# Optimization experiments

Measured on AMD Instinct MI355X. Metric: run time of the kernel, lower is better.

## Reference

```python
import jax, jax.numpy as jnp
import numpy as np

NUM_HEADS = 16

def setup_inputs() -> dict:
    key = jax.random.key(0)
    ks = jax.random.split(key, 10)
    B, S, D = 2, 2048, 1024
    q = jax.random.normal(ks[0], (B, S, D), dtype=jnp.float32)
    k = jax.random.normal(ks[1], (B, S, D), dtype=jnp.float32)
    v = jax.random.normal(ks[2], (B, S, D), dtype=jnp.float32)
    mask = jax.random.randint(ks[3], (B, S), 0, 2, dtype=jnp.int32)
    scale = 0.02
    Wq = jax.random.normal(ks[4], (D, D), dtype=jnp.float32) * scale
    bq = jax.random.normal(ks[5], (D,), dtype=jnp.float32) * scale
    Wk = jax.random.normal(ks[6], (D, D), dtype=jnp.float32) * scale
    bk = jax.random.normal(ks[7], (D,), dtype=jnp.float32) * scale
    Wv = jax.random.normal(ks[8], (D, D), dtype=jnp.float32) * scale
    bv = jax.random.normal(ks[9], (D,), dtype=jnp.float32) * scale
    return {"q": q, "k": k, "v": v, "mask": mask,
            "Wq": Wq, "bq": bq, "Wk": Wk, "bk": bk, "Wv": Wv, "bv": bv}


def reference(q, k, v, mask, Wq, bq, Wk, bk, Wv, bv):
    B, S, D = q.shape
    H = NUM_HEADS
    dh = D // H
    # per-head split along last dim == reshape to (B, S, H, dh)
    Qh = (q @ Wq + bq).reshape(B, S, H, dh)
    Kh = (k @ Wk + bk).reshape(B, S, H, dh)
    Vh = (v @ Wv + bv).reshape(B, S, H, dh)
    # NOTE: original scales by sqrt(10), not sqrt(dim_per_head)
    scores = jnp.einsum('bqhd,bkhd->bhqk', Qh, Kh) / jnp.sqrt(jnp.float32(10.0))
    # mask [B,S] masks key positions; masked_fill replaces with -1e9
    scores = jnp.where(mask[:, None, None, :] == 0, jnp.float32(-1e9), scores)
    probs = jax.nn.softmax(scores, axis=-1)
    out = jnp.einsum('bhqk,bkhd->bqhd', probs, Vh).reshape(B, S, D)
    return out
```

## Files before the change

kernel.cpp:

```cpp
#include <hip/hip_runtime.h>
#include <hip/hip_bf16.h>

typedef __attribute__((ext_vector_type(8))) short short8;
typedef __attribute__((ext_vector_type(4))) float f32x4;

#define SC_L2E 0.4561727848849353f

#if __has_builtin(__builtin_amdgcn_exp2f)
#define EXP2F __builtin_amdgcn_exp2f
#else
#define EXP2F exp2f
#endif

static __device__ __forceinline__ void gload16(const void* g, void* l) {
  __builtin_amdgcn_global_load_lds((const __attribute__((address_space(1))) void*)g,
                                   (__attribute__((address_space(3))) void*)l, 16, 0, 0);
}

__global__ void k_cvt(const float* __restrict__ q, const float* __restrict__ kk,
                      const float* __restrict__ v, __hip_bfloat16* __restrict__ xb,
                      const float* __restrict__ Wq, const float* __restrict__ Wk,
                      const float* __restrict__ Wv, __hip_bfloat16* __restrict__ wt,
                      const int* __restrict__ mask, float* __restrict__ bias2) {
  __shared__ float T[64][65];
  if (blockIdx.x < 6144) {
    const size_t i = ((size_t)blockIdx.x * 256 + threadIdx.x) * 8;
    const int t = (int)(i >> 22);
    const float* src = (t == 0) ? q : (t == 1) ? kk : v;
    const size_t off = i & 4194303u;
    float4 f0 = *(const float4*)(src + off);
    float4 f1 = *(const float4*)(src + off + 4);
    union { short8 s; __hip_bfloat16 h[8]; } u;
    u.h[0] = __float2bfloat16(f0.x); u.h[1] = __float2bfloat16(f0.y);
    u.h[2] = __float2bfloat16(f0.z); u.h[3] = __float2bfloat16(f0.w);
    u.h[4] = __float2bfloat16(f1.x); u.h[5] = __float2bfloat16(f1.y);
    u.h[6] = __float2bfloat16(f1.z); u.h[7] = __float2bfloat16(f1.w);
    *(short8*)((char*)xb + i * 2) = u.s;
    return;
  }
  const int idx2 = blockIdx.x - 6144;
  const int z = idx2 >> 8;
  const int r2 = idx2 & 255;
  const int bxi = r2 & 15, byi = r2 >> 4;
  if (z == 0 && byi == 0) {
    const int idx = bxi * 256 + threadIdx.x;
    bias2[idx] = mask[idx] ? -12.0f : -1e30f;
  }
  const float* W = (z == 0) ? Wq : (z == 1) ? Wk : Wv;
  __hip_bfloat16* Wd = wt + (size_t)z * 1048576;
  const int n0 = bxi * 64, k0 = byi * 64;
  const int tx = threadIdx.x & 63, ty = threadIdx.x >> 6;
#pragma unroll
  for (int r = 0; r < 16; ++r)
    T[ty + r * 4][tx] = W[(size_t)(k0 + ty + r * 4) * 1024 + n0 + tx];
  __syncthreads();
#pragma unroll
  for (int r = 0; r < 16; ++r)
    Wd[(size_t)(n0 + ty + r * 4) * 1024 + k0 + tx] = __float2bfloat16(T[tx][ty + r * 4]);
}

__global__ __launch_bounds__(256) void k_proj(
    const __hip_bfloat16* __restrict__ xb, const __hip_bfloat16* __restrict__ wt,
    const float* __restrict__ bq, const float* __restrict__ bk, const float* __restrict__ bv,
    __hip_bfloat16* __restrict__ Qb, __hip_bfloat16* __restrict__ Kb,
    __hip_bfloat16* __restrict__ Vt) {
  __shared__ char smem[32768];
  char* As = smem;
  char* Bs = smem + 16384;
  const int orig = blockIdx.x;
  const int xcd = orig & 7, idx = orig >> 3;
  const int by = xcd * 4 + (idx & 3);
  const int bx = (idx >> 2) & 7;
  const int t = idx >> 5;
  const char* X = (const char*)(xb + (size_t)t * 4194304);
  const char* W = (const char*)(wt + (size_t)t * 1048576);
  const float* bias = (t == 0) ? bq : (t == 1) ? bk : bv;
  const int m0 = by * 128, n0 = bx * 128;
  const int tid = threadIdx.x, w = tid >> 6, lane = tid & 63;
  const int l15 = lane & 15, g = lane >> 4;
  const int l8 = lane >> 3, l7 = lane & 7;
  const int vswz = ((l7 ^ l8) << 4);
  const int wm = (w >> 1) * 64, wn = (w & 1) * 64;
  f32x4 acc[4][4];
#pragma unroll
  for (int i = 0; i < 4; ++i)
#pragma unroll
    for (int j = 0; j < 4; ++j) acc[i][j] = (f32x4){0.f, 0.f, 0.f, 0.f};

  for (int k0 = 0; k0 < 2048; k0 += 128) {
    __syncthreads();
#pragma unroll
    for (int j = 0; j < 4; ++j) {
      const int ch = w * 4 + j;
      gload16(X + (size_t)(m0 + ch * 8 + l8) * 2048 + k0 + vswz, As + ch * 1024);
      gload16(W + (size_t)(n0 + ch * 8 + l8) * 2048 + k0 + vswz, Bs + ch * 1024);
    }
    __syncthreads();
#pragma unroll
    for (int kk = 0; kk < 2; ++kk) {
      short8 af[4], bf_[4];
#pragma unroll
      for (int mt = 0; mt < 4; ++mt) {
        const int row = wm + mt * 16 + l15;
        af[mt] = *(const short8*)(As + row * 128 + ((kk * 64 + g * 16) ^ ((row & 7) << 4)));
      }
#pragma unroll
      for (int nt = 0; nt < 4; ++nt) {
        const int row = wn + nt * 16 + l15;
        bf_[nt] = *(const short8*)(Bs + row * 128 + ((kk * 64 + g * 16) ^ ((row & 7) << 4)));
      }
#pragma unroll
      for (int mt = 0; mt < 4; ++mt)
#pragma unroll
        for (int nt = 0; nt < 4; ++nt)
          acc[mt][nt] = __builtin_amdgcn_mfma_f32_16x16x32_bf16(af[mt], bf_[nt], acc[mt][nt], 0, 0, 0);
    }
  }

  float bv4[4];
#pragma unroll
  for (int nt = 0; nt < 4; ++nt) bv4[nt] = bias[n0 + wn + nt * 16 + l15];

  if (t < 2) {
#pragma unroll
    for (int mt = 0; mt < 4; ++mt) {
#pragma unroll
      for (int nt = 0; nt < 4; ++nt) {
        const int feat = n0 + wn + nt * 16 + l15;
        const int h = feat >> 6, d = feat & 63;
#pragma unroll
        for (int r = 0; r < 4; ++r) {
          const int token = m0 + wm + mt * 16 + g * 4 + r;
          const int b = token >> 11, s = token & 2047;
          const float val = acc[mt][nt][r] + bv4[nt];
          const __hip_bfloat16 hb = __float2bfloat16(val);
          if (t == 0) Qb[((size_t)(b * 16 + h) * 2048 + s) * 64 + d] = hb;
          else        Kb[((size_t)(b * 16 + h) * 2048 + s) * 64 + d] = hb;
        }
      }
    }
  } else {
    __hip_bfloat16* T2 = (__hip_bfloat16*)smem;
    const int bb = m0 >> 11;
    const int s0 = m0 & 2047;
#pragma unroll
    for (int p = 0; p < 2; ++p) {
      __syncthreads();
      if ((w >> 1) == p) {
#pragma unroll
        for (int mt = 0; mt < 4; ++mt)
#pragma unroll
          for (int nt = 0; nt < 4; ++nt) {
            const int feat = wn + nt * 16 + l15;
#pragma unroll
            for (int r = 0; r < 4; ++r) {
              const int tok = mt * 16 + g * 4 + r;
              T2[feat * 64 + (tok ^ ((feat & 7) << 3))] =
                  __float2bfloat16(acc[mt][nt][r] + bv4[nt]);
            }
          }
      }
      __syncthreads();
#pragma unroll
      for (int sw = 0; sw < 4; ++sw) {
        const int row = sw * 32 + (tid >> 3);
        const int c = tid & 7;
        const short8 vchunk = *(const short8*)(smem + row * 128 + 16 * (c ^ (row & 7)));
        const int gfeat = n0 + row;
        const int hh = gfeat >> 6, dd = gfeat & 63;
        *(short8*)(Vt + ((size_t)((bb * 16 + hh) * 64 + dd)) * 2048 + s0 + p * 64 + c * 8) = vchunk;
      }
    }
  }
}

#define ATTN_BODY(CUR, NXT, PREF)                                              \
  {                                                                            \
    float4 mb[4];                                                              \
    _Pragma("unroll") for (int nt = 0; nt < 4; ++nt)                           \
        mb[nt] = *(const float4*)(mbp + (nt >> 1) * 32 + ((nt & 1) << 2) + g * 8); \
    mbp += 64;                                                                 \
    if (PREF) {                                                                \
      _Pragma("unroll") for (int j = 0; j < 2; ++j) {                          \
        gload16(kst[j], Ks[NXT] + (w * 2 + j) * 1024);                         \
        gload16(vst[j], Vs[NXT] + (w * 2 + j) * 1024);                         \
      }                                                                        \
    }                                                                          \
    kst[0] += 8192; kst[1] += 8192; vst[0] += 128; vst[1] += 128;              \
    f32x4 s_[4];                                                               \
    __builtin_amdgcn_s_setprio(1);                                             \
    _Pragma("unroll") for (int nt = 0; nt < 4; ++nt) {                         \
      s_[nt] = (f32x4){0.f, 0.f, 0.f, 0.f};                                    \
      const int key = nt * 16 + l15;                                           \
      _Pragma("unroll") for (int kc = 0; kc < 2; ++kc) {                       \
        const short8 kf = *(const short8*)(Ks[CUR] + key * 128 +               \
                           ((kc * 64 + g * 16) ^ ((key & 7) << 4)));           \
        s_[nt] = __builtin_amdgcn_mfma_f32_16x16x32_bf16(kf, aq[kc], s_[nt], 0, 0, 0); \
      }                                                                        \
    }                                                                          \
    __builtin_amdgcn_s_setprio(0);                                             \
    short8 pb8[2];                                                             \
    _Pragma("unroll") for (int c = 0; c < 2; ++c) {                            \
      union { short8 s8; __hip_bfloat16 hh[8]; } pu;                           \
      pu.hh[0] = __float2bfloat16(EXP2F(fmaf(s_[2*c][0], SC_L2E, mb[2*c].x))); \
      pu.hh[1] = __float2bfloat16(EXP2F(fmaf(s_[2*c][1], SC_L2E, mb[2*c].y))); \
      pu.hh[2] = __float2bfloat16(EXP2F(fmaf(s_[2*c][2], SC_L2E, mb[2*c].z))); \
      pu.hh[3] = __float2bfloat16(EXP2F(fmaf(s_[2*c][3], SC_L2E, mb[2*c].w))); \
      pu.hh[4] = __float2bfloat16(EXP2F(fmaf(s_[2*c+1][0], SC_L2E, mb[2*c+1].x))); \
      pu.hh[5] = __float2bfloat16(EXP2F(fmaf(s_[2*c+1][1], SC_L2E, mb[2*c+1].y))); \
      pu.hh[6] = __float2bfloat16(EXP2F(fmaf(s_[2*c+1][2], SC_L2E, mb[2*c+1].z))); \
      pu.hh[7] = __float2bfloat16(EXP2F(fmaf(s_[2*c+1][3], SC_L2E, mb[2*c+1].w))); \
      pb8[c] = pu.s8;                                                          \
    }                                                                          \
    __builtin_amdgcn_s_setprio(1);                                             \
    lacc = __builtin_amdgcn_mfma_f32_16x16x32_bf16(ones8, pb8[0], lacc, 0, 0, 0); \
    lacc = __builtin_amdgcn_mfma_f32_16x16x32_bf16(ones8, pb8[1], lacc, 0, 0, 0); \
    _Pragma("unroll") for (int dt = 0; dt < 4; ++dt) {                         \
      const int d = dt * 16 + l15;                                             \
      const int sw2 = (d & 7) << 4;                                            \
      f32x4 o = oaccT[dt];                                                     \
      const short8 v0 = *(const short8*)(Vs[CUR] + d * 128 + ((g * 16) ^ sw2)); \
      const short8 v1 = *(const short8*)(Vs[CUR] + d * 128 + ((64 + g * 16) ^ sw2)); \
      o = __builtin_amdgcn_mfma_f32_16x16x32_bf16(v0, pb8[0], o, 0, 0, 0);     \
      o = __builtin_amdgcn_mfma_f32_16x16x32_bf16(v1, pb8[1], o, 0, 0, 0);     \
      oaccT[dt] = o;                                                           \
    }                                                                          \
    __builtin_amdgcn_s_setprio(0);                                             \
    __syncthreads();                                                           \
  }

__global__ __launch_bounds__(256, 4) void k_attn(
    const __hip_bfloat16* __restrict__ Qb, const __hip_bfloat16* __restrict__ Kb,
    const __hip_bfloat16* __restrict__ Vt, const float* __restrict__ bias2,
    float* __restrict__ out) {
  __shared__ char Ks[2][8192];
  __shared__ char Vs[2][8192];
  const int orig = blockIdx.x;
  const int swz = (orig & 7) * 128 + (orig >> 3);
  const int bh = swz >> 5, qb = swz & 31;
  const int b = bh >> 4, h = bh & 15;
  const int tid = threadIdx.x, w = tid >> 6, lane = tid & 63;
  const int g = lane >> 4, l15 = lane & 15;
  const char* Qc = (const char*)(Qb + (size_t)bh * 131072);
  const char* Kc = (const char*)(Kb + (size_t)bh * 131072);
  const char* Vc = (const char*)(Vt + (size_t)bh * 131072);

  const int l8 = lane >> 3, l7 = lane & 7;
  const int vswz = ((l7 ^ l8) << 4);

  short8 aq[2];
  const int arow = qb * 64 + w * 16 + l15;
#pragma unroll
  for (int kc = 0; kc < 2; ++kc)
    aq[kc] = *(const short8*)(Qc + (size_t)arow * 128 + kc * 64 + g * 16);

  f32x4 oaccT[4];
#pragma unroll
  for (int i = 0; i < 4; ++i) oaccT[i] = (f32x4){0.f, 0.f, 0.f, 0.f};
  f32x4 lacc = (f32x4){0.f, 0.f, 0.f, 0.f};
  const short8 ones8 = {(short)0x3F80, (short)0x3F80, (short)0x3F80, (short)0x3F80,
                        (short)0x3F80, (short)0x3F80, (short)0x3F80, (short)0x3F80};

  const char* kst[2];
  const char* vst[2];
#pragma unroll
  for (int j = 0; j < 2; ++j) {
    const int ch = w * 2 + j;
    const int s = ch * 8 + l8;
    const int nt = s >> 4, gg = (s >> 2) & 3, rr = s & 3;
    const int kap = (nt >> 1) * 32 + gg * 8 + ((nt & 1) << 2) + rr;
    kst[j] = Kc + (size_t)kap * 128 + vswz;
    vst[j] = Vc + (size_t)s * 4096 + vswz;
    gload16(kst[j], Ks[0] + ch * 1024);
    gload16(vst[j], Vs[0] + ch * 1024);
    kst[j] += 8192;
    vst[j] += 128;
  }
  __syncthreads();

  const float* mbp = bias2 + b * 2048;
  for (int kt = 0; kt < 32; kt += 2) {
    ATTN_BODY(0, 1, true)
    ATTN_BODY(1, 0, (kt + 1 < 31))
  }

  const float rl = 1.0f / lacc[0];
  float* orow = out + ((size_t)(b * 2048 + arow)) * 1024 + h * 64;
#pragma unroll
  for (int dt = 0; dt < 4; ++dt) {
    float4 st;
    st.x = oaccT[dt][0] * rl; st.y = oaccT[dt][1] * rl;
    st.z = oaccT[dt][2] * rl; st.w = oaccT[dt][3] * rl;
    *(float4*)(orow + dt * 16 + g * 4) = st;
  }
}

extern "C" void kernel_launch(void* const* d_in, const int* in_sizes, int n_in,
                              void* d_out, int out_size, void* d_ws, size_t ws_size,
                              hipStream_t stream) {
  const float* q   = (const float*)d_in[0];
  const float* k   = (const float*)d_in[1];
  const float* v   = (const float*)d_in[2];
  const int* mask  = (const int*)d_in[3];
  const float* Wq  = (const float*)d_in[4];
  const float* bq  = (const float*)d_in[5];
  const float* Wk  = (const float*)d_in[6];
  const float* bk  = (const float*)d_in[7];
  const float* Wv  = (const float*)d_in[8];
  const float* bv  = (const float*)d_in[9];
  float* out = (float*)d_out;
  char* ws = (char*)d_ws;
  __hip_bfloat16* Xb = (__hip_bfloat16*)(ws);
  __hip_bfloat16* Wt = (__hip_bfloat16*)(ws + 25165824);
  __hip_bfloat16* Qb = (__hip_bfloat16*)(ws + 31457280);
  __hip_bfloat16* Kb = (__hip_bfloat16*)(ws + 39845888);
  __hip_bfloat16* Vt = (__hip_bfloat16*)(ws + 48234496);
  float* bias2      = (float*)(ws + 56623104);

  k_cvt<<<dim3(6912), dim3(256), 0, stream>>>(q, k, v, Xb, Wq, Wk, Wv, Wt, mask, bias2);
  k_proj<<<dim3(768), dim3(256), 0, stream>>>(Xb, Wt, bq, bk, bv, Qb, Kb, Vt);
  k_attn<<<dim3(1024), dim3(256), 0, stream>>>(Qb, Kb, Vt, bias2, out);
}
```

Measured before the change: 109.8 us.

## Double attention query tile to 128 rows with 8 waves per block

The attention kernel now launches 512 blocks of 512 threads. Each block covers 128 query rows instead of 64, and the K/V tile loads are spread over 8 waves, one 16-byte chunk per wave instead of two. This halves the total K/V global-to-LDS traffic and the number of blocks streaming the same head's keys and values. In exchange, more waves share each barrier per tile, and there are fewer blocks to spread across the CUs.

```diff
diff --git a/kernel.cpp b/kernel.cpp
--- a/kernel.cpp
+++ b/kernel.cpp
@@ -181,12 +181,10 @@
         mb[nt] = *(const float4*)(mbp + (nt >> 1) * 32 + ((nt & 1) << 2) + g * 8); \
     mbp += 64;                                                                 \
     if (PREF) {                                                                \
-      _Pragma("unroll") for (int j = 0; j < 2; ++j) {                          \
-        gload16(kst[j], Ks[NXT] + (w * 2 + j) * 1024);                         \
-        gload16(vst[j], Vs[NXT] + (w * 2 + j) * 1024);                         \
-      }                                                                        \
+      gload16(kst, Ks[NXT] + w * 1024);                                        \
+      gload16(vst, Vs[NXT] + w * 1024);                                        \
     }                                                                          \
-    kst[0] += 8192; kst[1] += 8192; vst[0] += 128; vst[1] += 128;              \
+    kst += 8192; vst += 128;                                                   \
     f32x4 s_[4];                                                               \
     __builtin_amdgcn_s_setprio(1);                                             \
     _Pragma("unroll") for (int nt = 0; nt < 4; ++nt) {                         \
@@ -229,15 +227,15 @@
     __syncthreads();                                                           \
   }
 
-__global__ __launch_bounds__(256, 4) void k_attn(
+__global__ __launch_bounds__(512, 2) void k_attn(
     const __hip_bfloat16* __restrict__ Qb, const __hip_bfloat16* __restrict__ Kb,
     const __hip_bfloat16* __restrict__ Vt, const float* __restrict__ bias2,
     float* __restrict__ out) {
   __shared__ char Ks[2][8192];
   __shared__ char Vs[2][8192];
   const int orig = blockIdx.x;
-  const int swz = (orig & 7) * 128 + (orig >> 3);
-  const int bh = swz >> 5, qb = swz & 31;
+  const int swz = (orig & 7) * 64 + (orig >> 3);
+  const int bh = swz >> 4, qb = swz & 15;
   const int b = bh >> 4, h = bh & 15;
   const int tid = threadIdx.x, w = tid >> 6, lane = tid & 63;
   const int g = lane >> 4, l15 = lane & 15;
@@ -249,7 +247,7 @@
   const int vswz = ((l7 ^ l8) << 4);
 
   short8 aq[2];
-  const int arow = qb * 64 + w * 16 + l15;
+  const int arow = qb * 128 + w * 16 + l15;
 #pragma unroll
   for (int kc = 0; kc < 2; ++kc)
     aq[kc] = *(const short8*)(Qc + (size_t)arow * 128 + kc * 64 + g * 16);
@@ -261,21 +259,15 @@
   const short8 ones8 = {(short)0x3F80, (short)0x3F80, (short)0x3F80, (short)0x3F80,
                         (short)0x3F80, (short)0x3F80, (short)0x3F80, (short)0x3F80};
 
-  const char* kst[2];
-  const char* vst[2];
-#pragma unroll
-  for (int j = 0; j < 2; ++j) {
-    const int ch = w * 2 + j;
-    const int s = ch * 8 + l8;
-    const int nt = s >> 4, gg = (s >> 2) & 3, rr = s & 3;
-    const int kap = (nt >> 1) * 32 + gg * 8 + ((nt & 1) << 2) + rr;
-    kst[j] = Kc + (size_t)kap * 128 + vswz;
-    vst[j] = Vc + (size_t)s * 4096 + vswz;
-    gload16(kst[j], Ks[0] + ch * 1024);
-    gload16(vst[j], Vs[0] + ch * 1024);
-    kst[j] += 8192;
-    vst[j] += 128;
-  }
+  const int s = w * 8 + l8;
+  const int nt0 = s >> 4, gg = (s >> 2) & 3, rr = s & 3;
+  const int kap = (nt0 >> 1) * 32 + gg * 8 + ((nt0 & 1) << 2) + rr;
+  const char* kst = Kc + (size_t)kap * 128 + vswz;
+  const char* vst = Vc + (size_t)s * 4096 + vswz;
+  gload16(kst, Ks[0] + w * 1024);
+  gload16(vst, Vs[0] + w * 1024);
+  kst += 8192;
+  vst += 128;
   __syncthreads();
 
   const float* mbp = bias2 + b * 2048;
@@ -319,5 +311,5 @@
 
   k_cvt<<<dim3(6912), dim3(256), 0, stream>>>(q, k, v, Xb, Wq, Wk, Wv, Wt, mask, bias2);
   k_proj<<<dim3(768), dim3(256), 0, stream>>>(Xb, Wt, bq, bk, bv, Qb, Kb, Vt);
-  k_attn<<<dim3(1024), dim3(256), 0, stream>>>(Qb, Kb, Vt, bias2, out);
-}
+  k_attn<<<dim3(512), dim3(512), 0, stream>>>(Qb, Kb, Vt, bias2, out);
+}
```

Result: faster. 104.4 us (-5.0%).

## Process two query tiles per wave and triple-buffer K/V loads in attention

Applied to the files above, without the earlier changes.

Each wave now handles 32 query rows (two 16-row tiles) instead of 16, so each K and V fragment read from LDS feeds twice as many MFMAs, and the grid is halved to 512 blocks. K/V staging goes from double to triple buffering. The full __syncthreads is replaced by an explicit vmcnt wait plus s_barrier so one prefetch stays in flight. This raises register pressure (launch bounds lowered to 2 waves per SIMD) and LDS use, and reduces the number of blocks available to fill the GPU.

```diff
diff --git a/kernel.cpp b/kernel.cpp
--- a/kernel.cpp
+++ b/kernel.cpp
@@ -174,70 +174,81 @@
   }
 }
 
-#define ATTN_BODY(CUR, NXT, PREF)                                              \
+#define ATTN_BODY(CUR, PRF, DOPREF, SYNC)                                      \
   {                                                                            \
     float4 mb[4];                                                              \
     _Pragma("unroll") for (int nt = 0; nt < 4; ++nt)                           \
         mb[nt] = *(const float4*)(mbp + (nt >> 1) * 32 + ((nt & 1) << 2) + g * 8); \
     mbp += 64;                                                                 \
-    if (PREF) {                                                                \
+    __builtin_amdgcn_sched_barrier(0);       \
+    if (DOPREF) {                                                              \
       _Pragma("unroll") for (int j = 0; j < 2; ++j) {                          \
-        gload16(kst[j], Ks[NXT] + (w * 2 + j) * 1024);                         \
-        gload16(vst[j], Vs[NXT] + (w * 2 + j) * 1024);                         \
+        gload16(kst[j], Ks[PRF] + (w * 2 + j) * 1024);                         \
+        gload16(vst[j], Vs[PRF] + (w * 2 + j) * 1024);                         \
       }                                                                        \
     }                                                                          \
     kst[0] += 8192; kst[1] += 8192; vst[0] += 128; vst[1] += 128;              \
-    f32x4 s_[4];                                                               \
+    f32x4 sA[4], sB[4];                                                        \
     __builtin_amdgcn_s_setprio(1);                                             \
     _Pragma("unroll") for (int nt = 0; nt < 4; ++nt) {                         \
-      s_[nt] = (f32x4){0.f, 0.f, 0.f, 0.f};                                    \
       const int key = nt * 16 + l15;                                           \
-      _Pragma("unroll") for (int kc = 0; kc < 2; ++kc) {                       \
-        const short8 kf = *(const short8*)(Ks[CUR] + key * 128 +               \
-                           ((kc * 64 + g * 16) ^ ((key & 7) << 4)));           \
-        s_[nt] = __builtin_amdgcn_mfma_f32_16x16x32_bf16(kf, aq[kc], s_[nt], 0, 0, 0); \
+      const int ksw = (key & 7) << 4;                                          \
+      const short8 kf0 = *(const short8*)(Ks[CUR] + key * 128 + ((g * 16) ^ ksw)); \
+      const short8 kf1 = *(const short8*)(Ks[CUR] + key * 128 + ((64 + g * 16) ^ ksw)); \
+      f32x4 z = (f32x4){0.f, 0.f, 0.f, 0.f};                                   \
+      sA[nt] = __builtin_amdgcn_mfma_f32_16x16x32_bf16(kf0, aq[0][0], z, 0, 0, 0); \
+      sA[nt] = __builtin_amdgcn_mfma_f32_16x16x32_bf16(kf1, aq[0][1], sA[nt], 0, 0, 0); \
+      sB[nt] = __builtin_amdgcn_mfma_f32_16x16x32_bf16(kf0, aq[1][0], z, 0, 0, 0); \
+      sB[nt] = __builtin_amdgcn_mfma_f32_16x16x32_bf16(kf1, aq[1][1], sB[nt], 0, 0, 0); \
+    }                                                                          \
+    __builtin_amdgcn_s_setprio(0);                                             \
+    short8 pbA[2], pbB[2];                                                     \
+    _Pragma("unroll") for (int c = 0; c < 2; ++c) {                            \
+      union { short8 s8; __hip_bfloat16 hh[8]; } pa, pb;                       \
+      _Pragma("unroll") for (int e = 0; e < 8; ++e) {                          \
+        const int nt = 2 * c + (e >> 2);                                       \
+        const float mbe = (e & 3) == 0 ? mb[nt].x : (e & 3) == 1 ? mb[nt].y :  \
+                          (e & 3) == 2 ? mb[nt].z : mb[nt].w;                  \
+        pa.hh[e] = __float2bfloat16(EXP2F(fmaf(sA[nt][e & 3], SC_L2E, mbe)));  \
+        pb.hh[e] = __float2bfloat16(EXP2F(fmaf(sB[nt][e & 3], SC_L2E, mbe)));  \
       }                                                                        \
-    }                                                                          \
-    __builtin_amdgcn_s_setprio(0);                                             \
-    short8 pb8[2];                                                             \
-    _Pragma("unroll") for (int c = 0; c < 2; ++c) {                            \
-      union { short8 s8; __hip_bfloat16 hh[8]; } pu;                           \
-      pu.hh[0] = __float2bfloat16(EXP2F(fmaf(s_[2*c][0], SC_L2E, mb[2*c].x))); \
-      pu.hh[1] = __float2bfloat16(EXP2F(fmaf(s_[2*c][1], SC_L2E, mb[2*c].y))); \
-      pu.hh[2] = __float2bfloat16(EXP2F(fmaf(s_[2*c][2], SC_L2E, mb[2*c].z))); \
-      pu.hh[3] = __float2bfloat16(EXP2F(fmaf(s_[2*c][3], SC_L2E, mb[2*c].w))); \
-      pu.hh[4] = __float2bfloat16(EXP2F(fmaf(s_[2*c+1][0], SC_L2E, mb[2*c+1].x))); \
-      pu.hh[5] = __float2bfloat16(EXP2F(fmaf(s_[2*c+1][1], SC_L2E, mb[2*c+1].y))); \
-      pu.hh[6] = __float2bfloat16(EXP2F(fmaf(s_[2*c+1][2], SC_L2E, mb[2*c+1].z))); \
-      pu.hh[7] = __float2bfloat16(EXP2F(fmaf(s_[2*c+1][3], SC_L2E, mb[2*c+1].w))); \
-      pb8[c] = pu.s8;                                                          \
+      pbA[c] = pa.s8; pbB[c] = pb.s8;                                          \
     }                                                                          \
     __builtin_amdgcn_s_setprio(1);                                             \
-    lacc = __builtin_amdgcn_mfma_f32_16x16x32_bf16(ones8, pb8[0], lacc, 0, 0, 0); \
-    lacc = __builtin_amdgcn_mfma_f32_16x16x32_bf16(ones8, pb8[1], lacc, 0, 0, 0); \
+    laccA = __builtin_amdgcn_mfma_f32_16x16x32_bf16(ones8, pbA[0], laccA, 0, 0, 0); \
+    laccA = __builtin_amdgcn_mfma_f32_16x16x32_bf16(ones8, pbA[1], laccA, 0, 0, 0); \
+    laccB = __builtin_amdgcn_mfma_f32_16x16x32_bf16(ones8, pbB[0], laccB, 0, 0, 0); \
+    laccB = __builtin_amdgcn_mfma_f32_16x16x32_bf16(ones8, pbB[1], laccB, 0, 0, 0); \
     _Pragma("unroll") for (int dt = 0; dt < 4; ++dt) {                         \
       const int d = dt * 16 + l15;                                             \
       const int sw2 = (d & 7) << 4;                                            \
-      f32x4 o = oaccT[dt];                                                     \
       const short8 v0 = *(const short8*)(Vs[CUR] + d * 128 + ((g * 16) ^ sw2)); \
       const short8 v1 = *(const short8*)(Vs[CUR] + d * 128 + ((64 + g * 16) ^ sw2)); \
-      o = __builtin_amdgcn_mfma_f32_16x16x32_bf16(v0, pb8[0], o, 0, 0, 0);     \
-      o = __builtin_amdgcn_mfma_f32_16x16x32_bf16(v1, pb8[1], o, 0, 0, 0);     \
-      oaccT[dt] = o;                                                           \
+      f32x4 oa = oaccA[dt], ob = oaccB[dt];                                    \
+      oa = __builtin_amdgcn_mfma_f32_16x16x32_bf16(v0, pbA[0], oa, 0, 0, 0);   \
+      oa = __builtin_amdgcn_mfma_f32_16x16x32_bf16(v1, pbA[1], oa, 0, 0, 0);   \
+      ob = __builtin_amdgcn_mfma_f32_16x16x32_bf16(v0, pbB[0], ob, 0, 0, 0);   \
+      ob = __builtin_amdgcn_mfma_f32_16x16x32_bf16(v1, pbB[1], ob, 0, 0, 0);   \
+      oaccA[dt] = oa; oaccB[dt] = ob;                                          \
     }                                                                          \
     __builtin_amdgcn_s_setprio(0);                                             \
-    __syncthreads();                                                           \
-  }
-
-__global__ __launch_bounds__(256, 4) void k_attn(
+    if (SYNC == 4) { asm volatile("s_waitcnt vmcnt(4)" ::: "memory"); }        \
+    else if (SYNC == 0) { asm volatile("s_waitcnt vmcnt(0)" ::: "memory"); }   \
+    if (SYNC >= 0) {                                                           \
+      __builtin_amdgcn_s_barrier();                                            \
+      __builtin_amdgcn_sched_barrier(0);                                       \
+    }                                                                          \
+  }
+
+__global__ __launch_bounds__(256, 2) void k_attn(
     const __hip_bfloat16* __restrict__ Qb, const __hip_bfloat16* __restrict__ Kb,
     const __hip_bfloat16* __restrict__ Vt, const float* __restrict__ bias2,
     float* __restrict__ out) {
-  __shared__ char Ks[2][8192];
-  __shared__ char Vs[2][8192];
+  __shared__ char Ks[3][8192];
+  __shared__ char Vs[3][8192];
   const int orig = blockIdx.x;
-  const int swz = (orig & 7) * 128 + (orig >> 3);
-  const int bh = swz >> 5, qb = swz & 31;
+  const int swz = (orig & 7) * 64 + (orig >> 3);
+  const int bh = swz >> 4, qb = swz & 15;
   const int b = bh >> 4, h = bh & 15;
   const int tid = threadIdx.x, w = tid >> 6, lane = tid & 63;
   const int g = lane >> 4, l15 = lane & 15;
@@ -248,16 +259,22 @@
   const int l8 = lane >> 3, l7 = lane & 7;
   const int vswz = ((l7 ^ l8) << 4);
 
-  short8 aq[2];
-  const int arow = qb * 64 + w * 16 + l15;
-#pragma unroll
-  for (int kc = 0; kc < 2; ++kc)
-    aq[kc] = *(const short8*)(Qc + (size_t)arow * 128 + kc * 64 + g * 16);
-
-  f32x4 oaccT[4];
-#pragma unroll
-  for (int i = 0; i < 4; ++i) oaccT[i] = (f32x4){0.f, 0.f, 0.f, 0.f};
-  f32x4 lacc = (f32x4){0.f, 0.f, 0.f, 0.f};
+  short8 aq[2][2];
+  const int arow0 = qb * 128 + w * 32 + l15;
+#pragma unroll
+  for (int qt = 0; qt < 2; ++qt)
+#pragma unroll
+    for (int kc = 0; kc < 2; ++kc)
+      aq[qt][kc] = *(const short8*)(Qc + (size_t)(arow0 + qt * 16) * 128 + kc * 64 + g * 16);
+
+  f32x4 oaccA[4], oaccB[4];
+#pragma unroll
+  for (int i = 0; i < 4; ++i) {
+    oaccA[i] = (f32x4){0.f, 0.f, 0.f, 0.f};
+    oaccB[i] = (f32x4){0.f, 0.f, 0.f, 0.f};
+  }
+  f32x4 laccA = (f32x4){0.f, 0.f, 0.f, 0.f};
+  f32x4 laccB = (f32x4){0.f, 0.f, 0.f, 0.f};
   const short8 ones8 = {(short)0x3F80, (short)0x3F80, (short)0x3F80, (short)0x3F80,
                         (short)0x3F80, (short)0x3F80, (short)0x3F80, (short)0x3F80};
 
@@ -267,31 +284,46 @@
   for (int j = 0; j < 2; ++j) {
     const int ch = w * 2 + j;
     const int s = ch * 8 + l8;
-    const int nt = s >> 4, gg = (s >> 2) & 3, rr = s & 3;
-    const int kap = (nt >> 1) * 32 + gg * 8 + ((nt & 1) << 2) + rr;
+    const int nt0 = s >> 4, gg = (s >> 2) & 3, rr = s & 3;
+    const int kap = (nt0 >> 1) * 32 + gg * 8 + ((nt0 & 1) << 2) + rr;
     kst[j] = Kc + (size_t)kap * 128 + vswz;
     vst[j] = Vc + (size_t)s * 4096 + vswz;
-    gload16(kst[j], Ks[0] + ch * 1024);
-    gload16(vst[j], Vs[0] + ch * 1024);
-    kst[j] += 8192;
-    vst[j] += 128;
-  }
-  __syncthreads();
+  }
+#pragma unroll
+  for (int tpre = 0; tpre < 2; ++tpre) {
+#pragma unroll
+    for (int j = 0; j < 2; ++j) {
+      gload16(kst[j], Ks[tpre] + (w * 2 + j) * 1024);
+      gload16(vst[j], Vs[tpre] + (w * 2 + j) * 1024);
+    }
+    kst[0] += 8192; kst[1] += 8192; vst[0] += 128; vst[1] += 128;
+  }
+  asm volatile("s_waitcnt vmcnt(4)" ::: "memory");
+  __builtin_amdgcn_s_barrier();
+  __builtin_amdgcn_sched_barrier(0);
 
   const float* mbp = bias2 + b * 2048;
-  for (int kt = 0; kt < 32; kt += 2) {
-    ATTN_BODY(0, 1, true)
-    ATTN_BODY(1, 0, (kt + 1 < 31))
-  }
-
-  const float rl = 1.0f / lacc[0];
-  float* orow = out + ((size_t)(b * 2048 + arow)) * 1024 + h * 64;
+  for (int k = 0; k < 10; ++k) {
+    ATTN_BODY(0, 2, 1, 4)
+    ATTN_BODY(1, 0, 1, 4)
+    ATTN_BODY(2, 1, 1, 4)
+  }
+  ATTN_BODY(0, 2, 0, 0)
+  ATTN_BODY(1, 0, 0, -1)
+
+  const float rlA = 1.0f / laccA[0];
+  const float rlB = 1.0f / laccB[0];
+  float* orowA = out + ((size_t)(b * 2048 + arow0)) * 1024 + h * 64;
+  float* orowB = orowA + 16 * 1024;
 #pragma unroll
   for (int dt = 0; dt < 4; ++dt) {
-    float4 st;
-    st.x = oaccT[dt][0] * rl; st.y = oaccT[dt][1] * rl;
-    st.z = oaccT[dt][2] * rl; st.w = oaccT[dt][3] * rl;
-    *(float4*)(orow + dt * 16 + g * 4) = st;
+    float4 stA, stB;
+    stA.x = oaccA[dt][0] * rlA; stA.y = oaccA[dt][1] * rlA;
+    stA.z = oaccA[dt][2] * rlA; stA.w = oaccA[dt][3] * rlA;
+    stB.x = oaccB[dt][0] * rlB; stB.y = oaccB[dt][1] * rlB;
+    stB.z = oaccB[dt][2] * rlB; stB.w = oaccB[dt][3] * rlB;
+    *(float4*)(orowA + dt * 16 + g * 4) = stA;
+    *(float4*)(orowB + dt * 16 + g * 4) = stB;
   }
 }
 
@@ -319,5 +351,5 @@
 
   k_cvt<<<dim3(6912), dim3(256), 0, stream>>>(q, k, v, Xb, Wq, Wk, Wv, Wt, mask, bias2);
   k_proj<<<dim3(768), dim3(256), 0, stream>>>(Xb, Wt, bq, bk, bv, Qb, Kb, Vt);
-  k_attn<<<dim3(1024), dim3(256), 0, stream>>>(Qb, Kb, Vt, bias2, out);
-}
+  k_attn<<<dim3(512), dim3(256), 0, stream>>>(Qb, Kb, Vt, bias2, out);
+}
```

Result: faster. 102.4 us (-6.7%).
